# Performance work log

Measured on AMD Instinct MI355X. Metric: run time of the kernel, lower is better.

The kernel has to match this reference:

```python
import jax, jax.numpy as jnp
import numpy as np

EPS = 1e-5

def _ln(x, g, b):
    mu = jnp.mean(x, axis=-1, keepdims=True)
    var = jnp.mean(jnp.square(x - mu), axis=-1, keepdims=True)
    return (x - mu) * jax.lax.rsqrt(var + EPS) * g + b

def setup_inputs() -> dict:
    BS, LN, FS = 64, 256, 512
    H, OUT, ATT, L = 1024, 128, 256, 8
    key = jax.random.key(0)
    ks = jax.random.split(key, 8)
    s = 0.02
    inp = {
        "x": jax.random.normal(ks[0], (BS, LN, FS), jnp.float32),
        # fc stem
        "ln0_g": jnp.ones((FS,), jnp.float32),
        "ln0_b": jnp.zeros((FS,), jnp.float32),
        "W0": jax.random.normal(ks[1], (FS, H), jnp.float32) * s,
        "b0": jnp.zeros((H,), jnp.float32),
        # residual blocks (stacked)
        "res_ln_g": jnp.ones((L, H), jnp.float32),
        "res_ln_b": jnp.zeros((L, H), jnp.float32),
        "res_W": jax.random.normal(ks[2], (L, H, H), jnp.float32) * s,
        "res_b": jnp.zeros((L, H), jnp.float32),
        # fc head
        "lnf_g": jnp.ones((H,), jnp.float32),
        "lnf_b": jnp.zeros((H,), jnp.float32),
        "Wf": jax.random.normal(ks[3], (H, OUT), jnp.float32) * s,
        "bf": jnp.zeros((OUT,), jnp.float32),
        # attention MLP over time axis
        "a_ln1_g": jnp.ones((LN + 1,), jnp.float32),
        "a_ln1_b": jnp.zeros((LN + 1,), jnp.float32),
        "Wa1": jax.random.normal(ks[4], (LN + 1, ATT), jnp.float32) * s,
        "ba1": jnp.zeros((ATT,), jnp.float32),
        "a_ln2_g": jnp.ones((ATT,), jnp.float32),
        "a_ln2_b": jnp.zeros((ATT,), jnp.float32),
        "Wa2": jax.random.normal(ks[5], (ATT, LN), jnp.float32) * s,
        "ba2": jnp.zeros((LN,), jnp.float32),
    }
    return inp

def reference(x, ln0_g, ln0_b, W0, b0, res_ln_g, res_ln_b, res_W, res_b,
              lnf_g, lnf_b, Wf, bf, a_ln1_g, a_ln1_b, Wa1, ba1,
              a_ln2_g, a_ln2_b, Wa2, ba2):
    # fc trunk (dropout is identity in eval)
    h = jax.nn.relu(_ln(x, ln0_g, ln0_b) @ W0 + b0)          # [bs, ln, H]
    for i in range(res_W.shape[0]):
        h = h + jax.nn.relu(_ln(h, res_ln_g[i], res_ln_b[i]) @ res_W[i] + res_b[i])
    fc_out = _ln(h, lnf_g, lnf_b) @ Wf + bf                  # [bs, ln, out]

    # attention: batched over (bs, out) instead of python loop
    mean = jnp.mean(fc_out, axis=1, keepdims=True)           # [bs, 1, out]
    t = jnp.concatenate([fc_out, mean], axis=1).transpose(0, 2, 1)  # [bs, out, ln+1]
    a = jax.nn.relu(_ln(t, a_ln1_g, a_ln1_b) @ Wa1 + ba1)    # [bs, out, att]
    w = _ln(a, a_ln2_g, a_ln2_b) @ Wa2 + ba2                 # [bs, out, ln]
    w = jax.nn.softmax(w, axis=2).transpose(0, 2, 1)         # [bs, ln, out]

    # einsum('ijk,ijk->ik')
    return jnp.sum(fc_out * w, axis=1)                        # [bs, out]
```

## Files before the change

### kernel.cpp

```cpp
#include <hip/hip_runtime.h>
#include <hip/hip_bf16.h>
#include <stdint.h>

#define EPSV 1e-5f

typedef int i32x4 __attribute__((ext_vector_type(4)));

#define QINV_X 15.875f
#define SA_X   0.062992126f
#define QINV_H 5.2916667f
#define SA_H   0.188976378f

__device__ __forceinline__ void gload_lds16(const void* g, void* l) {
    __builtin_amdgcn_global_load_lds(
        (const __attribute__((address_space(1))) uint32_t*)g,
        (__attribute__((address_space(3))) uint32_t*)l, 16, 0, 0);
}

__device__ __forceinline__ float block_sum256(float v, float* red) {
#pragma unroll
    for (int off = 32; off; off >>= 1) v += __shfl_down(v, off);
    int lane = threadIdx.x & 63, w = threadIdx.x >> 6;
    __syncthreads();
    if (lane == 0) red[w] = v;
    __syncthreads();
    return red[0] + red[1] + red[2] + red[3];
}

__global__ __launch_bounds__(256)
void pack_x0(const float* __restrict__ X, uint8_t* __restrict__ Aq,
             float* __restrict__ S0, int D) {
    __shared__ float red[4];
    int row = blockIdx.x;
    const float* x = X + (size_t)row * D;
    int tid = threadIdx.x;
    int nvec = D >> 2;

    float s = 0.f, sq = 0.f;
    for (int i = tid; i < nvec; i += 256) {
        float4 v = ((const float4*)x)[i];
        s += v.x + v.y + v.z + v.w;
        sq += v.x * v.x + v.y * v.y + v.z * v.z + v.w * v.w;
    }
    float ts = block_sum256(s, red);
    float tq = block_sum256(sq, red);
    if (tid == 0) { S0[2 * row] = ts; S0[2 * row + 1] = tq; }

    uint8_t* arow = Aq + (size_t)row * ((size_t)D * 2);
    for (int i = tid; i < nvec; i += 256) {
        float4 v = ((const float4*)x)[i];
        float vals[4] = { v.x, v.y, v.z, v.w };
        uint32_t u1 = 0, u2 = 0;
#pragma unroll
        for (int j = 0; j < 4; ++j) {
            float qv = vals[j] * QINV_X;
            float q1 = rintf(qv);
            q1 = fminf(fmaxf(q1, -127.f), 127.f);
            float q2 = fminf(fmaxf(rintf((qv - q1) * 128.f), -127.f), 127.f);
            u1 |= ((uint32_t)((int)q1 & 0xFF)) << (8 * j);
            u2 |= ((uint32_t)((int)q2 & 0xFF)) << (8 * j);
        }
        int kt = i >> 4;
        int o = (i & 15) * 4;
        *(uint32_t*)(arow + kt * 128 + o) = u1;
        *(uint32_t*)(arow + kt * 128 + 64 + o) = u2;
    }
}

__global__ __launch_bounds__(256)
void wprep_part(const float* __restrict__ W, const float* __restrict__ g,
                const float* __restrict__ lb, float* __restrict__ pA,
                float* __restrict__ pC, float* __restrict__ pD, int K, int N) {
    int n = blockIdx.y * 256 + threadIdx.x;
    int kp = blockIdx.x;
    if (n >= N) return;
    int kc = K >> 3, k0 = kp * kc;
    float ma = 0.f, cs = 0.f, ds = 0.f;
    for (int k = k0; k < k0 + kc; ++k) {
        float w = W[(size_t)k * N + n];
        float gw = g[k] * w;
        ma = fmaxf(ma, fabsf(gw));
        cs += gw;
        ds = fmaf(lb[k], w, ds);
    }
    pA[kp * N + n] = ma;
    pC[kp * N + n] = cs;
    pD[kp * N + n] = ds;
}

__global__ __launch_bounds__(256)
void wprep_fin(const float* __restrict__ pA, const float* __restrict__ pC,
               const float* __restrict__ pD, const float* __restrict__ bias,
               float* __restrict__ sB, float* __restrict__ csum,
               float* __restrict__ d, int N) {
    int n = blockIdx.x * 256 + threadIdx.x;
    if (n >= N) return;
    float m = 0.f, cs = 0.f, ds = 0.f;
#pragma unroll
    for (int kp = 0; kp < 8; ++kp) {
        m = fmaxf(m, pA[kp * N + n]);
        cs += pC[kp * N + n];
        ds += pD[kp * N + n];
    }
    m = fmaxf(m, 1e-30f);
    sB[n] = m * (1.f / 127.f);
    csum[n] = cs;
    d[n] = ds + bias[n];
}

__global__ __launch_bounds__(64)
void conv_wq(const float* __restrict__ W, const float* __restrict__ g,
             const float* __restrict__ sB, uint8_t* __restrict__ Wq,
             int K, int N) {
    int n = blockIdx.x * 64 + threadIdx.x;
    int kt = blockIdx.y;
    if (n >= N) return;
    float inv = 1.f / sB[n];
    uint32_t u1[16], u2[16];
#pragma unroll 4
    for (int o = 0; o < 16; ++o) {
        uint32_t a = 0, bq = 0;
#pragma unroll
        for (int j = 0; j < 4; ++j) {
            int k = kt * 64 + o * 4 + j;
            float q = g[k] * W[(size_t)k * N + n] * inv;
            float q1 = rintf(q);
            float q2 = rintf((q - q1) * 128.f);
            a |= ((uint32_t)((int)q1 & 0xFF)) << (8 * j);
            bq |= ((uint32_t)((int)q2 & 0xFF)) << (8 * j);
        }
        u1[o] = a; u2[o] = bq;
    }
    uint8_t* wrow = Wq + (size_t)n * ((size_t)K * 2) + kt * 128;
    uint4* dd = (uint4*)wrow;
    const uint4* p1 = (const uint4*)u1;
    const uint4* p2 = (const uint4*)u2;
    dd[0] = p1[0]; dd[1] = p1[1]; dd[2] = p1[2]; dd[3] = p1[3];
    dd[4] = p2[0]; dd[5] = p2[1]; dd[6] = p2[2]; dd[7] = p2[3];
}

__global__ __launch_bounds__(256)
void wprep_part_rw(const float* __restrict__ rW, const float* __restrict__ g8,
                   const float* __restrict__ lb8, float* __restrict__ pA,
                   float* __restrict__ pC, float* __restrict__ pD) {
    int c = blockIdx.y * 256 + threadIdx.x;
    int kp = blockIdx.x;
    int layer = c >> 10, n = c & 1023;
    const float* W = rW + ((size_t)layer << 20);
    const float* g = g8 + layer * 1024;
    const float* lb = lb8 + layer * 1024;
    int k0 = kp * 128;
    float ma = 0.f, cs = 0.f, ds = 0.f;
    for (int k = k0; k < k0 + 128; ++k) {
        float w = W[(size_t)k * 1024 + n];
        float gw = g[k] * w;
        ma = fmaxf(ma, fabsf(gw));
        cs += gw;
        ds = fmaf(lb[k], w, ds);
    }
    pA[kp * 8192 + c] = ma;
    pC[kp * 8192 + c] = cs;
    pD[kp * 8192 + c] = ds;
}

__global__ __launch_bounds__(256)
void wprep_fin_rw(const float* __restrict__ pA, const float* __restrict__ pC,
                  const float* __restrict__ pD, const float* __restrict__ rb,
                  float* __restrict__ sB, float* __restrict__ csum,
                  float* __restrict__ d) {
    int c = blockIdx.x * 256 + threadIdx.x;
    float m = 0.f, cs = 0.f, ds = 0.f;
#pragma unroll
    for (int kp = 0; kp < 8; ++kp) {
        m = fmaxf(m, pA[kp * 8192 + c]);
        cs += pC[kp * 8192 + c];
        ds += pD[kp * 8192 + c];
    }
    m = fmaxf(m, 1e-30f);
    sB[c] = m * (1.f / 127.f);
    csum[c] = cs;
    d[c] = ds + rb[c];
}

__global__ __launch_bounds__(64)
void conv_wq_rw(const float* __restrict__ rW, const float* __restrict__ g8,
                const float* __restrict__ sB, uint8_t* __restrict__ Wq) {
    int c = blockIdx.x * 64 + threadIdx.x;
    int kt = blockIdx.y;
    int layer = c >> 10, n = c & 1023;
    const float* W = rW + ((size_t)layer << 20);
    const float* g = g8 + layer * 1024;
    float inv = 1.f / sB[c];
    uint32_t u1[16], u2[16];
#pragma unroll 4
    for (int o = 0; o < 16; ++o) {
        uint32_t a = 0, bq = 0;
#pragma unroll
        for (int j = 0; j < 4; ++j) {
            int k = kt * 64 + o * 4 + j;
            float q = g[k] * W[(size_t)k * 1024 + n] * inv;
            float q1 = rintf(q);
            float q2 = rintf((q - q1) * 128.f);
            a |= ((uint32_t)((int)q1 & 0xFF)) << (8 * j);
            bq |= ((uint32_t)((int)q2 & 0xFF)) << (8 * j);
        }
        u1[o] = a; u2[o] = bq;
    }
    uint8_t* wrow = Wq + ((size_t)layer << 21) + (size_t)n * 2048 + kt * 128;
    uint4* dd = (uint4*)wrow;
    const uint4* p1 = (const uint4*)u1;
    const uint4* p2 = (const uint4*)u2;
    dd[0] = p1[0]; dd[1] = p1[1]; dd[2] = p1[2]; dd[3] = p1[3];
    dd[4] = p2[0]; dd[5] = p2[1]; dd[6] = p2[2]; dd[7] = p2[3];
}

template <int MODE, bool KSPLIT = false>
__global__ __launch_bounds__(512, 4)
void gemm_fold(const uint8_t* __restrict__ Aq, const uint8_t* __restrict__ Bq,
               const float* __restrict__ sB, const float* __restrict__ csum,
               const float* __restrict__ dvec, const float* __restrict__ Sin,
               float* __restrict__ Sout, uint8_t* __restrict__ AqOut,
               float* __restrict__ C, float SA, int M, int N, int K) {
    __shared__ char Abuf[2][16384];
    __shared__ char Bbuf[2][16384];

    const int tid = threadIdx.x;
    const int lane = tid & 63;
    const int wv = tid >> 6;
    const int wr = wv >> 1;
    const int wc = wv & 1;

    int m0, n0, nt;
    size_t kbyte0;
    float* Cout;
    if constexpr (KSPLIT) {
        m0 = blockIdx.x * 128;
        n0 = 0;
        int half = K >> 1;
        nt = half >> 6;
        kbyte0 = (size_t)blockIdx.y * half * 2;
        Cout = C + (size_t)blockIdx.y * M * N;
    } else {
        int lid = blockIdx.y * gridDim.x + blockIdx.x;
        int nwg = gridDim.x * gridDim.y;
        int chunk = nwg >> 3;
        int swz = (lid & 7) * chunk + (lid >> 3);
        int nIdx = swz % gridDim.y;
        int mIdx = swz / gridDim.y;
        m0 = mIdx * 128; n0 = nIdx * 128;
        nt = K >> 6;
        kbyte0 = 0;
        Cout = C;
    }

    const size_t rowB = (size_t)K * 2;

    int arow[2], aq[2];
#pragma unroll
    for (int i = 0; i < 2; ++i) {
        int s = i * 512 + tid;
        arow[i] = s >> 3;
        aq[i] = (s & 7) ^ (arow[i] & 7);
    }

    i32x4 accP[2][4] = {};
    i32x4 accQ[2][4] = {};

#pragma unroll
    for (int i = 0; i < 2; ++i) {
        gload_lds16((const char*)Aq + (size_t)(m0 + arow[i]) * rowB + kbyte0 + aq[i] * 16,
                    Abuf[0] + (i * 512 + tid) * 16);
        gload_lds16((const char*)Bq + (size_t)(n0 + arow[i]) * rowB + kbyte0 + aq[i] * 16,
                    Bbuf[0] + (i * 512 + tid) * 16);
    }
    __syncthreads();

    int p = 0;
    const int g = lane >> 4;
    const int rr = lane & 15;

    for (int kt = 0; kt < nt; ++kt) {
        if (kt + 1 < nt) {
            const size_t koff = kbyte0 + (size_t)(kt + 1) * 128;
#pragma unroll
            for (int i = 0; i < 2; ++i) {
                gload_lds16((const char*)Aq + (size_t)(m0 + arow[i]) * rowB + koff + aq[i] * 16,
                            Abuf[p ^ 1] + (i * 512 + tid) * 16);
                gload_lds16((const char*)Bq + (size_t)(n0 + arow[i]) * rowB + koff + aq[i] * 16,
                            Bbuf[p ^ 1] + (i * 512 + tid) * 16);
            }
        }

        const char* Ab = Abuf[p];
        const char* Bb = Bbuf[p];

        i32x4 a1[2], b1[4];
#pragma unroll
        for (int m = 0; m < 2; ++m) {
            int rA = wr * 32 + m * 16 + rr;
            a1[m] = *(const i32x4*)(Ab + rA * 128 + ((g ^ (rA & 7)) * 16));
        }
#pragma unroll
        for (int n = 0; n < 4; ++n) {
            int rB = wc * 64 + n * 16 + rr;
            b1[n] = *(const i32x4*)(Bb + rB * 128 + ((g ^ (rB & 7)) * 16));
        }
#pragma unroll
        for (int m = 0; m < 2; ++m)
#pragma unroll
            for (int n = 0; n < 4; ++n)
                accP[m][n] = __builtin_amdgcn_mfma_i32_16x16x64_i8(a1[m], b1[n], accP[m][n], 0, 0, 0);

        {
            i32x4 b2[4];
#pragma unroll
            for (int n = 0; n < 4; ++n) {
                int rB = wc * 64 + n * 16 + rr;
                b2[n] = *(const i32x4*)(Bb + rB * 128 + (((g + 4) ^ (rB & 7)) * 16));
            }
#pragma unroll
            for (int m = 0; m < 2; ++m)
#pragma unroll
                for (int n = 0; n < 4; ++n)
                    accQ[m][n] = __builtin_amdgcn_mfma_i32_16x16x64_i8(a1[m], b2[n], accQ[m][n], 0, 0, 0);
        }
        {
            i32x4 a2[2];
#pragma unroll
            for (int m = 0; m < 2; ++m) {
                int rA = wr * 32 + m * 16 + rr;
                a2[m] = *(const i32x4*)(Ab + rA * 128 + (((g + 4) ^ (rA & 7)) * 16));
            }
#pragma unroll
            for (int m = 0; m < 2; ++m)
#pragma unroll
                for (int n = 0; n < 4; ++n)
                    accQ[m][n] = __builtin_amdgcn_mfma_i32_16x16x64_i8(a2[m], b1[n], accQ[m][n], 0, 0, 0);
        }

        __syncthreads();
        p ^= 1;
    }

    const int rg = lane >> 4;
    const int cl = lane & 15;
    const float invK = 1.f / (float)K;

    float sbv[4], csv[4], dvv[4];
#pragma unroll
    for (int n = 0; n < 4; ++n) {
        int c = n0 + wc * 64 + n * 16 + cl;
        sbv[n] = sB[c] * SA;
        if (KSPLIT && blockIdx.y != 0) { csv[n] = 0.f; dvv[n] = 0.f; }
        else { csv[n] = csum[c]; dvv[n] = dvec[c]; }
    }

#pragma unroll
    for (int m = 0; m < 2; ++m) {
#pragma unroll
        for (int j = 0; j < 4; ++j) {
            int r = m0 + wr * 32 + m * 16 + rg * 4 + j;
            float mu = Sin[2 * r] * invK;
            float var = Sin[2 * r + 1] * invK - mu * mu;
            float rstd = rsqrtf(var + EPSV);
            float rs = 0.f, rq = 0.f;
#pragma unroll
            for (int n = 0; n < 4; ++n) {
                int c = n0 + wc * 64 + n * 16 + cl;
                float accv = (float)accP[m][n][j] + 0.0078125f * (float)accQ[m][n][j];
                float y = rstd * (sbv[n] * accv - mu * csv[n]) + dvv[n];
                if (MODE == 2) {
                    Cout[(size_t)r * N + c] = y;
                } else {
                    float* hp = &C[(size_t)r * N + c];
                    float hn = fmaxf(y, 0.f);
                    if (MODE == 1) hn += *hp;
                    *hp = hn;
                    float qv = hn * QINV_H;
                    float q1 = rintf(qv);
                    q1 = fminf(fmaxf(q1, -127.f), 127.f);
                    float q2 = fminf(fmaxf(rintf((qv - q1) * 128.f), -127.f), 127.f);
                    uint8_t* po = AqOut + (size_t)r * ((size_t)N * 2) + ((c >> 6) << 7) + (c & 63);
                    po[0] = (uint8_t)((int)q1 & 0xFF);
                    po[64] = (uint8_t)((int)q2 & 0xFF);
                    rs += hn;
                    rq += hn * hn;
                }
            }
            if (MODE != 2) {
#pragma unroll
                for (int mm = 1; mm < 16; mm <<= 1) {
                    rs += __shfl_xor(rs, mm);
                    rq += __shfl_xor(rq, mm);
                }
                if (cl == 0) {
                    atomicAdd(&Sout[2 * r], rs);
                    atomicAdd(&Sout[2 * r + 1], rq);
                }
            }
        }
    }
}

template <bool MAXOP>
__device__ __forceinline__ void red8(const float* v, float* out, float (*scr)[4]) {
    int lane = threadIdx.x & 63, wv = threadIdx.x >> 6, tid = threadIdx.x;
#pragma unroll
    for (int oo = 0; oo < 8; ++oo) {
        float r = v[oo];
#pragma unroll
        for (int m = 1; m < 64; m <<= 1) {
            float t = __shfl_xor(r, m);
            r = MAXOP ? fmaxf(r, t) : r + t;
        }
        if (lane == 0) scr[oo][wv] = r;
    }
    __syncthreads();
    if (tid < 8) {
        float a = scr[tid][0], b = scr[tid][1], c = scr[tid][2], d = scr[tid][3];
        out[tid] = MAXOP ? fmaxf(fmaxf(a, b), fmaxf(c, d)) : (a + b + c + d);
    }
    __syncthreads();
}

__global__ __launch_bounds__(256, 4)
void attn_g8(const float* __restrict__ fc01,
             const float* __restrict__ g1, const float* __restrict__ b1,
             const float* __restrict__ Wa1, const float* __restrict__ ba1,
             const float* __restrict__ g2, const float* __restrict__ b2,
             const float* __restrict__ Wa2, const float* __restrict__ ba2,
             float* __restrict__ out) {
    __shared__ float buf[257][12];
    __shared__ float scr[8][4];
    __shared__ float sS[8], sQ[8], sO[8];

    const int R128 = 16384 * 128;
    int bs = blockIdx.x >> 4;
    int o0 = (blockIdx.x & 15) * 8;
    int tid = threadIdx.x;
    int jgrp = tid >> 2;
    int kp = tid & 3;

    float vv[8], tmp[8];
    size_t base = (size_t)(bs * 256 + tid) * 128 + o0;
    const float4* fp0 = (const float4*)(fc01 + base);
    const float4* fp1 = (const float4*)(fc01 + R128 + base);
#pragma unroll
    for (int q = 0; q < 2; ++q) {
        float4 t0 = fp0[q];
        float4 t1 = fp1[q];
        vv[4 * q] = t0.x + t1.x; vv[4 * q + 1] = t0.y + t1.y;
        vv[4 * q + 2] = t0.z + t1.z; vv[4 * q + 3] = t0.w + t1.w;
    }

#pragma unroll
    for (int oo = 0; oo < 8; ++oo) tmp[oo] = vv[oo] * vv[oo];
    red8<false>(vv, sS, scr);
    red8<false>(tmp, sQ, scr);

    float gl = g1[tid], bl = b1[tid];
#pragma unroll
    for (int oo = 0; oo < 8; ++oo) {
        float s = sS[oo], q = sQ[oo];
        float mean = s * (1.f / 256.f);
        float mu = (s + mean) * (1.f / 257.f);
        float var = (q + mean * mean) * (1.f / 257.f) - mu * mu;
        float rstd = rsqrtf(var + EPSV);
        tmp[oo] = (vv[oo] - mu) * rstd * gl + bl;
    }
#pragma unroll
    for (int q = 0; q < 2; ++q)
        *(float4*)&buf[tid][4 * q] = *(float4*)&tmp[4 * q];
    if (tid < 8) {
        int oo = tid;
        float s = sS[oo], q = sQ[oo];
        float mean = s * (1.f / 256.f);
        float mu = (s + mean) * (1.f / 257.f);
        float var = (q + mean * mean) * (1.f / 257.f) - mu * mu;
        float rstd = rsqrtf(var + EPSV);
        buf[256][oo] = (mean - mu) * rstd * g1[256] + b1[256];
    }
    __syncthreads();

    float acc1[8][4] = {};
#pragma unroll 2
    for (int i = 0; i < 64; ++i) {
        int k = 4 * i + kp;
        float4 w4 = *(const float4*)&Wa1[(size_t)k * 256 + jgrp * 4];
        float4 t0 = *(const float4*)&buf[k][0];
        float4 t1 = *(const float4*)&buf[k][4];
        float bv[8] = { t0.x, t0.y, t0.z, t0.w, t1.x, t1.y, t1.z, t1.w };
#pragma unroll
        for (int oo = 0; oo < 8; ++oo) {
            acc1[oo][0] = fmaf(bv[oo], w4.x, acc1[oo][0]);
            acc1[oo][1] = fmaf(bv[oo], w4.y, acc1[oo][1]);
            acc1[oo][2] = fmaf(bv[oo], w4.z, acc1[oo][2]);
            acc1[oo][3] = fmaf(bv[oo], w4.w, acc1[oo][3]);
        }
    }
    if (kp == 0) {
        float4 w4 = *(const float4*)&Wa1[(size_t)256 * 256 + jgrp * 4];
#pragma unroll
        for (int oo = 0; oo < 8; ++oo) {
            float bv = buf[256][oo];
            acc1[oo][0] = fmaf(bv, w4.x, acc1[oo][0]);
            acc1[oo][1] = fmaf(bv, w4.y, acc1[oo][1]);
            acc1[oo][2] = fmaf(bv, w4.z, acc1[oo][2]);
            acc1[oo][3] = fmaf(bv, w4.w, acc1[oo][3]);
        }
    }
    float a_[8];
#pragma unroll
    for (int oo = 0; oo < 8; ++oo) {
#pragma unroll
        for (int jj = 0; jj < 4; ++jj) {
            acc1[oo][jj] += __shfl_xor(acc1[oo][jj], 1);
            acc1[oo][jj] += __shfl_xor(acc1[oo][jj], 2);
        }
        float v01 = (kp & 1) ? acc1[oo][1] : acc1[oo][0];
        float v23 = (kp & 1) ? acc1[oo][3] : acc1[oo][2];
        a_[oo] = (kp & 2) ? v23 : v01;
    }
    float bb = ba1[tid];
#pragma unroll
    for (int oo = 0; oo < 8; ++oo) a_[oo] = fmaxf(a_[oo] + bb, 0.f);

#pragma unroll
    for (int oo = 0; oo < 8; ++oo) tmp[oo] = a_[oo] * a_[oo];
    red8<false>(a_, sS, scr);
    red8<false>(tmp, sQ, scr);

    float g2l = g2[tid], b2l = b2[tid];
#pragma unroll
    for (int oo = 0; oo < 8; ++oo) {
        float mu2 = sS[oo] * (1.f / 256.f);
        float rstd2 = rsqrtf(sQ[oo] * (1.f / 256.f) - mu2 * mu2 + EPSV);
        tmp[oo] = (a_[oo] - mu2) * rstd2 * g2l + b2l;
    }
#pragma unroll
    for (int q = 0; q < 2; ++q)
        *(float4*)&buf[tid][4 * q] = *(float4*)&tmp[4 * q];
    __syncthreads();

    float acc2[8][4] = {};
#pragma unroll 2
    for (int i = 0; i < 64; ++i) {
        int k = 4 * i + kp;
        float4 w4 = *(const float4*)&Wa2[(size_t)k * 256 + jgrp * 4];
        float4 t0 = *(const float4*)&buf[k][0];
        float4 t1 = *(const float4*)&buf[k][4];
        float bv[8] = { t0.x, t0.y, t0.z, t0.w, t1.x, t1.y, t1.z, t1.w };
#pragma unroll
        for (int oo = 0; oo < 8; ++oo) {
            acc2[oo][0] = fmaf(bv[oo], w4.x, acc2[oo][0]);
            acc2[oo][1] = fmaf(bv[oo], w4.y, acc2[oo][1]);
            acc2[oo][2] = fmaf(bv[oo], w4.z, acc2[oo][2]);
            acc2[oo][3] = fmaf(bv[oo], w4.w, acc2[oo][3]);
        }
    }
    float w_[8];
#pragma unroll
    for (int oo = 0; oo < 8; ++oo) {
#pragma unroll
        for (int jj = 0; jj < 4; ++jj) {
            acc2[oo][jj] += __shfl_xor(acc2[oo][jj], 1);
            acc2[oo][jj] += __shfl_xor(acc2[oo][jj], 2);
        }
        float v01 = (kp & 1) ? acc2[oo][1] : acc2[oo][0];
        float v23 = (kp & 1) ? acc2[oo][3] : acc2[oo][2];
        w_[oo] = (kp & 2) ? v23 : v01;
    }
    float bb2 = ba2[tid];
#pragma unroll
    for (int oo = 0; oo < 8; ++oo) w_[oo] += bb2;

    red8<true>(w_, sO, scr);
    float e_[8];
#pragma unroll
    for (int oo = 0; oo < 8; ++oo) e_[oo] = __expf(w_[oo] - sO[oo]);
    red8<false>(e_, sS, scr);
#pragma unroll
    for (int oo = 0; oo < 8; ++oo) tmp[oo] = vv[oo] * e_[oo] / sS[oo];
    red8<false>(tmp, sQ, scr);
    if (tid < 8) out[bs * 128 + o0 + tid] = sQ[tid];
}

extern "C" void kernel_launch(void* const* d_in, const int* in_sizes, int n_in,
                              void* d_out, int out_size, void* d_ws, size_t ws_size,
                              hipStream_t stream) {
    const float* x      = (const float*)d_in[0];
    const float* ln0_g  = (const float*)d_in[1];
    const float* ln0_b  = (const float*)d_in[2];
    const float* W0     = (const float*)d_in[3];
    const float* b0     = (const float*)d_in[4];
    const float* rln_g  = (const float*)d_in[5];
    const float* rln_b  = (const float*)d_in[6];
    const float* rW     = (const float*)d_in[7];
    const float* rb     = (const float*)d_in[8];
    const float* lnf_g  = (const float*)d_in[9];
    const float* lnf_b  = (const float*)d_in[10];
    const float* Wf     = (const float*)d_in[11];
    const float* bf_    = (const float*)d_in[12];
    const float* ln1_g  = (const float*)d_in[13];
    const float* ln1_b  = (const float*)d_in[14];
    const float* Wa1    = (const float*)d_in[15];
    const float* ba1    = (const float*)d_in[16];
    const float* ln2_g  = (const float*)d_in[17];
    const float* ln2_b  = (const float*)d_in[18];
    const float* Wa2    = (const float*)d_in[19];
    const float* ba2    = (const float*)d_in[20];
    float* out = (float*)d_out;

    const size_t R = 16384;
    float*   h    = (float*)d_ws;
    uint8_t* AqX  = (uint8_t*)(h + R * 1024);
    uint8_t* Aq1  = AqX + R * 1024;
    uint8_t* Aq2  = Aq1 + R * 2048;
    float*   fc01 = (float*)(Aq2 + R * 2048);
    uint8_t* Wq0  = (uint8_t*)(fc01 + 2 * R * 128);
    uint8_t* WqR  = Wq0 + (size_t)1024 * 1024;
    uint8_t* Wqf  = WqR + (size_t)8 * 1024 * 2048;
    float*   stats = (float*)(Wqf + (size_t)128 * 2048);
    float*   sB0  = stats + 10 * R * 2;
    float*   cs0  = sB0 + 1024;
    float*   d0   = cs0 + 1024;
    float*   sBR  = d0 + 1024;
    float*   csR  = sBR + 8192;
    float*   dR   = csR + 8192;
    float*   sBf  = dR + 8192;
    float*   csf  = sBf + 128;
    float*   df   = csf + 128;
    float*   pA   = df + 128;
    float*   pC   = pA + 65536;
    float*   pD   = pC + 65536;

    hipMemsetAsync(stats, 0, 10 * R * 2 * sizeof(float), stream);

    wprep_part<<<dim3(8, 4), 256, 0, stream>>>(W0, ln0_g, ln0_b, pA, pC, pD, 512, 1024);
    wprep_fin<<<4, 256, 0, stream>>>(pA, pC, pD, b0, sB0, cs0, d0, 1024);
    conv_wq<<<dim3(16, 8), 64, 0, stream>>>(W0, ln0_g, sB0, Wq0, 512, 1024);

    wprep_part_rw<<<dim3(8, 32), 256, 0, stream>>>(rW, rln_g, rln_b, pA, pC, pD);
    wprep_fin_rw<<<32, 256, 0, stream>>>(pA, pC, pD, rb, sBR, csR, dR);
    conv_wq_rw<<<dim3(128, 16), 64, 0, stream>>>(rW, rln_g, sBR, WqR);

    wprep_part<<<dim3(8, 1), 256, 0, stream>>>(Wf, lnf_g, lnf_b, pA, pC, pD, 1024, 128);
    wprep_fin<<<1, 256, 0, stream>>>(pA, pC, pD, bf_, sBf, csf, df, 128);
    conv_wq<<<dim3(2, 16), 64, 0, stream>>>(Wf, lnf_g, sBf, Wqf, 1024, 128);

    pack_x0<<<R, 256, 0, stream>>>(x, AqX, stats, 512);

    gemm_fold<0><<<dim3(128, 8), 512, 0, stream>>>(
        AqX, Wq0, sB0, cs0, d0, stats, stats + R * 2, Aq1, h, SA_X,
        (int)R, 1024, 512);

    uint8_t* cur = Aq1;
    uint8_t* nxt = Aq2;
    for (int i = 0; i < 8; ++i) {
        gemm_fold<1><<<dim3(128, 8), 512, 0, stream>>>(
            cur, WqR + ((size_t)i << 21), sBR + i * 1024, csR + i * 1024, dR + i * 1024,
            stats + (size_t)(1 + i) * R * 2, stats + (size_t)(2 + i) * R * 2,
            nxt, h, SA_H, (int)R, 1024, 1024);
        uint8_t* t = cur; cur = nxt; nxt = t;
    }

    gemm_fold<2, true><<<dim3(128, 2), 512, 0, stream>>>(
        cur, Wqf, sBf, csf, df, stats + (size_t)9 * R * 2, nullptr, nullptr,
        fc01, SA_H, (int)R, 128, 1024);

    attn_g8<<<64 * 16, 256, 0, stream>>>(fc01, ln1_g, ln1_b, Wa1, ba1,
                                         ln2_g, ln2_b, Wa2, ba2, out);
}
```

Measured before the change: 1.009 ms.

## Move attention MLP GEMMs to int8 split-precision MFMA kernels

Replaces the monolithic fp32 FMA attention kernel with a pipeline: a pre-pass normalizes and quantizes each time-series row to two-level int8 (hi/lo bytes) with per-row scales, then an int8 MFMA GEMM computes the first projection with ReLU. A mid kernel applies the second layernorm and requantizes, a second int8 MFMA GEMM computes the logits, and a post kernel does the softmax-weighted reduction. Attention weights are quantized per column on device. This trades scalar FMA compute for matrix cores, at the cost of extra launches, intermediate global-memory traffic and some quantization error.

```diff
diff --git a/kernel.cpp b/kernel.cpp
--- a/kernel.cpp
+++ b/kernel.cpp
@@ -25,6 +25,25 @@
     if (lane == 0) red[w] = v;
     __syncthreads();
     return red[0] + red[1] + red[2] + red[3];
+}
+
+__device__ __forceinline__ float block_max256(float v, float* red) {
+#pragma unroll
+    for (int off = 32; off; off >>= 1) v = fmaxf(v, __shfl_down(v, off));
+    int lane = threadIdx.x & 63, w = threadIdx.x >> 6;
+    __syncthreads();
+    if (lane == 0) red[w] = v;
+    __syncthreads();
+    return fmaxf(fmaxf(red[0], red[1]), fmaxf(red[2], red[3]));
+}
+
+__device__ __forceinline__ void dq8(float v, float inv, uint8_t& q1o, uint8_t& q2o) {
+    float qv = v * inv;
+    float q1 = rintf(qv);
+    q1 = fminf(fmaxf(q1, -127.f), 127.f);
+    float q2 = fminf(fmaxf(rintf((qv - q1) * 128.f), -127.f), 127.f);
+    q1o = (uint8_t)((int)q1 & 0xFF);
+    q2o = (uint8_t)((int)q2 & 0xFF);
 }
 
 __global__ __launch_bounds__(256)
@@ -53,12 +72,10 @@
         uint32_t u1 = 0, u2 = 0;
 #pragma unroll
         for (int j = 0; j < 4; ++j) {
-            float qv = vals[j] * QINV_X;
-            float q1 = rintf(qv);
-            q1 = fminf(fmaxf(q1, -127.f), 127.f);
-            float q2 = fminf(fmaxf(rintf((qv - q1) * 128.f), -127.f), 127.f);
-            u1 |= ((uint32_t)((int)q1 & 0xFF)) << (8 * j);
-            u2 |= ((uint32_t)((int)q2 & 0xFF)) << (8 * j);
+            uint8_t a, b;
+            dq8(vals[j], QINV_X, a, b);
+            u1 |= ((uint32_t)a) << (8 * j);
+            u2 |= ((uint32_t)b) << (8 * j);
         }
         int kt = i >> 4;
         int o = (i & 15) * 4;
@@ -207,6 +224,63 @@
         u1[o] = a; u2[o] = bq;
     }
     uint8_t* wrow = Wq + ((size_t)layer << 21) + (size_t)n * 2048 + kt * 128;
+    uint4* dd = (uint4*)wrow;
+    const uint4* p1 = (const uint4*)u1;
+    const uint4* p2 = (const uint4*)u2;
+    dd[0] = p1[0]; dd[1] = p1[1]; dd[2] = p1[2]; dd[3] = p1[3];
+    dd[4] = p2[0]; dd[5] = p2[1]; dd[6] = p2[2]; dd[7] = p2[3];
+}
+
+__global__ __launch_bounds__(256)
+void wa_absmax(const float* __restrict__ W, float* __restrict__ part,
+               int K, int N) {
+    int n = blockIdx.y * 256 + threadIdx.x;
+    int kp = blockIdx.x;
+    if (n >= N) return;
+    int kc = (K + 7) >> 3;
+    int k0 = kp * kc;
+    int k1 = min(k0 + kc, K);
+    float m = 0.f;
+    for (int k = k0; k < k1; ++k)
+        m = fmaxf(m, fabsf(W[(size_t)k * N + n]));
+    part[kp * N + n] = m;
+}
+
+__global__ __launch_bounds__(256)
+void col_scale_s(const float* __restrict__ part, float* __restrict__ sB, int N) {
+    int n = blockIdx.x * 256 + threadIdx.x;
+    if (n >= N) return;
+    float m = 0.f;
+#pragma unroll
+    for (int kp = 0; kp < 8; ++kp) m = fmaxf(m, part[kp * N + n]);
+    m = fmaxf(m, 1e-30f);
+    sB[n] = m * (1.f / 127.f);
+}
+
+__global__ __launch_bounds__(64)
+void conv_wq_pad(const float* __restrict__ W, const float* __restrict__ sB,
+                 uint8_t* __restrict__ Wq, int Ktrue, int Kpad, int N) {
+    int n = blockIdx.x * 64 + threadIdx.x;
+    int kt = blockIdx.y;
+    if (n >= N) return;
+    float inv = 1.f / sB[n];
+    uint32_t u1[16], u2[16];
+#pragma unroll 4
+    for (int o = 0; o < 16; ++o) {
+        uint32_t a = 0, bq = 0;
+#pragma unroll
+        for (int j = 0; j < 4; ++j) {
+            int k = kt * 64 + o * 4 + j;
+            float w = (k < Ktrue) ? W[(size_t)k * N + n] : 0.f;
+            float q = w * inv;
+            float q1 = rintf(q);
+            float q2 = rintf((q - q1) * 128.f);
+            a |= ((uint32_t)((int)q1 & 0xFF)) << (8 * j);
+            bq |= ((uint32_t)((int)q2 & 0xFF)) << (8 * j);
+        }
+        u1[o] = a; u2[o] = bq;
+    }
+    uint8_t* wrow = Wq + (size_t)n * ((size_t)Kpad * 2) + kt * 128;
     uint4* dd = (uint4*)wrow;
     const uint4* p1 = (const uint4*)u1;
     const uint4* p2 = (const uint4*)u2;
@@ -402,6 +476,138 @@
     }
 }
 
+template <int MODE>
+__global__ __launch_bounds__(512, 4)
+void gemm_i8(const uint8_t* __restrict__ Aq, const uint8_t* __restrict__ Bq,
+             const float* __restrict__ sA, const float* __restrict__ sB,
+             const float* __restrict__ bias, float* __restrict__ C,
+             int M, int N, int K) {
+    __shared__ char Abuf[2][16384];
+    __shared__ char Bbuf[2][16384];
+
+    const int tid = threadIdx.x;
+    const int lane = tid & 63;
+    const int wv = tid >> 6;
+    const int wr = wv >> 1;
+    const int wc = wv & 1;
+
+    int lid = blockIdx.y * gridDim.x + blockIdx.x;
+    int nwg = gridDim.x * gridDim.y;
+    int chunk = nwg >> 3;
+    int swz = (lid & 7) * chunk + (lid >> 3);
+    int nIdx = swz % gridDim.y;
+    int mIdx = swz / gridDim.y;
+    const int m0 = mIdx * 128, n0 = nIdx * 128;
+    const int nt = K >> 6;
+    const size_t rowB = (size_t)K * 2;
+
+    int arow[2], aq[2];
+#pragma unroll
+    for (int i = 0; i < 2; ++i) {
+        int s = i * 512 + tid;
+        arow[i] = s >> 3;
+        aq[i] = (s & 7) ^ (arow[i] & 7);
+    }
+
+    i32x4 accP[2][4] = {};
+    i32x4 accQ[2][4] = {};
+
+#pragma unroll
+    for (int i = 0; i < 2; ++i) {
+        gload_lds16((const char*)Aq + (size_t)(m0 + arow[i]) * rowB + aq[i] * 16,
+                    Abuf[0] + (i * 512 + tid) * 16);
+        gload_lds16((const char*)Bq + (size_t)(n0 + arow[i]) * rowB + aq[i] * 16,
+                    Bbuf[0] + (i * 512 + tid) * 16);
+    }
+    __syncthreads();
+
+    int p = 0;
+    const int g = lane >> 4;
+    const int rr = lane & 15;
+
+    for (int kt = 0; kt < nt; ++kt) {
+        if (kt + 1 < nt) {
+            const size_t koff = (size_t)(kt + 1) * 128;
+#pragma unroll
+            for (int i = 0; i < 2; ++i) {
+                gload_lds16((const char*)Aq + (size_t)(m0 + arow[i]) * rowB + koff + aq[i] * 16,
+                            Abuf[p ^ 1] + (i * 512 + tid) * 16);
+                gload_lds16((const char*)Bq + (size_t)(n0 + arow[i]) * rowB + koff + aq[i] * 16,
+                            Bbuf[p ^ 1] + (i * 512 + tid) * 16);
+            }
+        }
+
+        const char* Ab = Abuf[p];
+        const char* Bb = Bbuf[p];
+
+        i32x4 a1[2], b1[4];
+#pragma unroll
+        for (int m = 0; m < 2; ++m) {
+            int rA = wr * 32 + m * 16 + rr;
+            a1[m] = *(const i32x4*)(Ab + rA * 128 + ((g ^ (rA & 7)) * 16));
+        }
+#pragma unroll
+        for (int n = 0; n < 4; ++n) {
+            int rB = wc * 64 + n * 16 + rr;
+            b1[n] = *(const i32x4*)(Bb + rB * 128 + ((g ^ (rB & 7)) * 16));
+        }
+#pragma unroll
+        for (int m = 0; m < 2; ++m)
+#pragma unroll
+            for (int n = 0; n < 4; ++n)
+                accP[m][n] = __builtin_amdgcn_mfma_i32_16x16x64_i8(a1[m], b1[n], accP[m][n], 0, 0, 0);
+
+        {
+            i32x4 b2[4];
+#pragma unroll
+            for (int n = 0; n < 4; ++n) {
+                int rB = wc * 64 + n * 16 + rr;
+                b2[n] = *(const i32x4*)(Bb + rB * 128 + (((g + 4) ^ (rB & 7)) * 16));
+            }
+#pragma unroll
+            for (int m = 0; m < 2; ++m)
+#pragma unroll
+                for (int n = 0; n < 4; ++n)
+                    accQ[m][n] = __builtin_amdgcn_mfma_i32_16x16x64_i8(a1[m], b2[n], accQ[m][n], 0, 0, 0);
+        }
+        {
+            i32x4 a2[2];
+#pragma unroll
+            for (int m = 0; m < 2; ++m) {
+                int rA = wr * 32 + m * 16 + rr;
+                a2[m] = *(const i32x4*)(Ab + rA * 128 + (((g + 4) ^ (rA & 7)) * 16));
+            }
+#pragma unroll
+            for (int m = 0; m < 2; ++m)
+#pragma unroll
+                for (int n = 0; n < 4; ++n)
+                    accQ[m][n] = __builtin_amdgcn_mfma_i32_16x16x64_i8(a2[m], b1[n], accQ[m][n], 0, 0, 0);
+        }
+
+        __syncthreads();
+        p ^= 1;
+    }
+
+#pragma unroll
+    for (int m = 0; m < 2; ++m) {
+        int rbase = m0 + wr * 32 + m * 16 + (lane >> 4) * 4;
+#pragma unroll
+        for (int n = 0; n < 4; ++n) {
+            int c = n0 + wc * 64 + n * 16 + (lane & 15);
+            float sbc = sB[c];
+            float bv = bias[c];
+#pragma unroll
+            for (int j = 0; j < 4; ++j) {
+                int r = rbase + j;
+                float v = sA[r] * sbc *
+                          ((float)accP[m][n][j] + 0.0078125f * (float)accQ[m][n][j]) + bv;
+                if (MODE == 0) v = fmaxf(v, 0.f);
+                C[(size_t)r * N + c] = v;
+            }
+        }
+    }
+}
+
 template <bool MAXOP>
 __device__ __forceinline__ void red8(const float* v, float* out, float (*scr)[4]) {
     int lane = threadIdx.x & 63, wv = threadIdx.x >> 6, tid = threadIdx.x;
@@ -423,25 +629,21 @@
     __syncthreads();
 }
 
-__global__ __launch_bounds__(256, 4)
-void attn_g8(const float* __restrict__ fc01,
-             const float* __restrict__ g1, const float* __restrict__ b1,
-             const float* __restrict__ Wa1, const float* __restrict__ ba1,
-             const float* __restrict__ g2, const float* __restrict__ b2,
-             const float* __restrict__ Wa2, const float* __restrict__ ba2,
-             float* __restrict__ out) {
-    __shared__ float buf[257][12];
+__global__ __launch_bounds__(256)
+void attn_pre(const float* __restrict__ fc01,
+              const float* __restrict__ g1, const float* __restrict__ b1,
+              uint8_t* __restrict__ AqT, float* __restrict__ sTn) {
     __shared__ float scr[8][4];
     __shared__ float sS[8], sQ[8], sO[8];
+    __shared__ float t256[8];
 
     const int R128 = 16384 * 128;
     int bs = blockIdx.x >> 4;
     int o0 = (blockIdx.x & 15) * 8;
     int tid = threadIdx.x;
-    int jgrp = tid >> 2;
-    int kp = tid & 3;
-
-    float vv[8], tmp[8];
+    int rbase = bs * 128 + o0;
+
+    float vv[8], tn[8], tmp[8];
     size_t base = (size_t)(bs * 256 + tid) * 128 + o0;
     const float4* fp0 = (const float4*)(fc01 + base);
     const float4* fp1 = (const float4*)(fc01 + R128 + base);
@@ -466,11 +668,9 @@
         float mu = (s + mean) * (1.f / 257.f);
         float var = (q + mean * mean) * (1.f / 257.f) - mu * mu;
         float rstd = rsqrtf(var + EPSV);
-        tmp[oo] = (vv[oo] - mu) * rstd * gl + bl;
-    }
-#pragma unroll
-    for (int q = 0; q < 2; ++q)
-        *(float4*)&buf[tid][4 * q] = *(float4*)&tmp[4 * q];
+        tn[oo] = (vv[oo] - mu) * rstd * gl + bl;
+        tmp[oo] = fabsf(tn[oo]);
+    }
     if (tid < 8) {
         int oo = tid;
         float s = sS[oo], q = sQ[oo];
@@ -478,111 +678,95 @@
         float mu = (s + mean) * (1.f / 257.f);
         float var = (q + mean * mean) * (1.f / 257.f) - mu * mu;
         float rstd = rsqrtf(var + EPSV);
-        buf[256][oo] = (mean - mu) * rstd * g1[256] + b1[256];
+        t256[oo] = (mean - mu) * rstd * g1[256] + b1[256];
+    }
+    red8<true>(tmp, sO, scr);
+    if (tid < 8) {
+        sO[tid] = fmaxf(fmaxf(sO[tid], fabsf(t256[tid])), 1e-30f);
+        sTn[rbase + tid] = sO[tid] * (1.f / 127.f);
     }
     __syncthreads();
 
-    float acc1[8][4] = {};
-#pragma unroll 2
-    for (int i = 0; i < 64; ++i) {
-        int k = 4 * i + kp;
-        float4 w4 = *(const float4*)&Wa1[(size_t)k * 256 + jgrp * 4];
-        float4 t0 = *(const float4*)&buf[k][0];
-        float4 t1 = *(const float4*)&buf[k][4];
-        float bv[8] = { t0.x, t0.y, t0.z, t0.w, t1.x, t1.y, t1.z, t1.w };
+#pragma unroll
+    for (int oo = 0; oo < 8; ++oo) {
+        float inv = 127.f / sO[oo];
+        uint8_t q1, q2;
+        dq8(tn[oo], inv, q1, q2);
+        uint8_t* po = AqT + (size_t)(rbase + oo) * 640 + ((tid >> 6) << 7) + (tid & 63);
+        po[0] = q1;
+        po[64] = q2;
+    }
+    if (tid < 64) {
 #pragma unroll
         for (int oo = 0; oo < 8; ++oo) {
-            acc1[oo][0] = fmaf(bv[oo], w4.x, acc1[oo][0]);
-            acc1[oo][1] = fmaf(bv[oo], w4.y, acc1[oo][1]);
-            acc1[oo][2] = fmaf(bv[oo], w4.z, acc1[oo][2]);
-            acc1[oo][3] = fmaf(bv[oo], w4.w, acc1[oo][3]);
-        }
-    }
-    if (kp == 0) {
-        float4 w4 = *(const float4*)&Wa1[(size_t)256 * 256 + jgrp * 4];
-#pragma unroll
-        for (int oo = 0; oo < 8; ++oo) {
-            float bv = buf[256][oo];
-            acc1[oo][0] = fmaf(bv, w4.x, acc1[oo][0]);
-            acc1[oo][1] = fmaf(bv, w4.y, acc1[oo][1]);
-            acc1[oo][2] = fmaf(bv, w4.z, acc1[oo][2]);
-            acc1[oo][3] = fmaf(bv, w4.w, acc1[oo][3]);
-        }
-    }
-    float a_[8];
-#pragma unroll
-    for (int oo = 0; oo < 8; ++oo) {
-#pragma unroll
-        for (int jj = 0; jj < 4; ++jj) {
-            acc1[oo][jj] += __shfl_xor(acc1[oo][jj], 1);
-            acc1[oo][jj] += __shfl_xor(acc1[oo][jj], 2);
-        }
-        float v01 = (kp & 1) ? acc1[oo][1] : acc1[oo][0];
-        float v23 = (kp & 1) ? acc1[oo][3] : acc1[oo][2];
-        a_[oo] = (kp & 2) ? v23 : v01;
-    }
-    float bb = ba1[tid];
-#pragma unroll
-    for (int oo = 0; oo < 8; ++oo) a_[oo] = fmaxf(a_[oo] + bb, 0.f);
-
-#pragma unroll
-    for (int oo = 0; oo < 8; ++oo) tmp[oo] = a_[oo] * a_[oo];
-    red8<false>(a_, sS, scr);
+            uint8_t q1 = 0, q2 = 0;
+            if (tid == 0) dq8(t256[oo], 127.f / sO[oo], q1, q2);
+            uint8_t* po = AqT + (size_t)(rbase + oo) * 640 + 512 + tid;
+            po[0] = q1;
+            po[64] = q2;
+        }
+    }
+}
+
+__global__ __launch_bounds__(256)
+void attn_mid(const float* __restrict__ A, const float* __restrict__ g2,
+              const float* __restrict__ b2, uint8_t* __restrict__ AqM,
+              float* __restrict__ sA2) {
+    __shared__ float red[4];
+    int r = blockIdx.x;
+    int tid = threadIdx.x;
+    float a = A[(size_t)r * 256 + tid];
+    float s = block_sum256(a, red);
+    float q = block_sum256(a * a, red);
+    float mu = s * (1.f / 256.f);
+    float rstd = rsqrtf(q * (1.f / 256.f) - mu * mu + EPSV);
+    float an = (a - mu) * rstd * g2[tid] + b2[tid];
+    float mx = block_max256(fabsf(an), red);
+    mx = fmaxf(mx, 1e-30f);
+    if (tid == 0) sA2[r] = mx * (1.f / 127.f);
+    uint8_t q1, q2;
+    dq8(an, 127.f / mx, q1, q2);
+    uint8_t* po = AqM + (size_t)r * 512 + ((tid >> 6) << 7) + (tid & 63);
+    po[0] = q1;
+    po[64] = q2;
+}
+
+__global__ __launch_bounds__(256)
+void attn_post(const float* __restrict__ fc01, const float* __restrict__ W2,
+               float* __restrict__ out) {
+    __shared__ float scr[8][4];
+    __shared__ float sS[8], sQ[8], sO[8];
+
+    const int R128 = 16384 * 128;
+    int bs = blockIdx.x >> 4;
+    int o0 = (blockIdx.x & 15) * 8;
+    int tid = threadIdx.x;
+    int rbase = bs * 128 + o0;
+
+    float vv[8], wv[8], tmp[8];
+    size_t base = (size_t)(bs * 256 + tid) * 128 + o0;
+    const float4* fp0 = (const float4*)(fc01 + base);
+    const float4* fp1 = (const float4*)(fc01 + R128 + base);
+#pragma unroll
+    for (int q = 0; q < 2; ++q) {
+        float4 t0 = fp0[q];
+        float4 t1 = fp1[q];
+        vv[4 * q] = t0.x + t1.x; vv[4 * q + 1] = t0.y + t1.y;
+        vv[4 * q + 2] = t0.z + t1.z; vv[4 * q + 3] = t0.w + t1.w;
+    }
+#pragma unroll
+    for (int oo = 0; oo < 8; ++oo)
+        wv[oo] = W2[(size_t)(rbase + oo) * 256 + tid];
+
+    red8<true>(wv, sO, scr);
+    float e_[8];
+#pragma unroll
+    for (int oo = 0; oo < 8; ++oo) e_[oo] = __expf(wv[oo] - sO[oo]);
+    red8<false>(e_, sS, scr);
+#pragma unroll
+    for (int oo = 0; oo < 8; ++oo) tmp[oo] = vv[oo] * e_[oo];
     red8<false>(tmp, sQ, scr);
-
-    float g2l = g2[tid], b2l = b2[tid];
-#pragma unroll
-    for (int oo = 0; oo < 8; ++oo) {
-        float mu2 = sS[oo] * (1.f / 256.f);
-        float rstd2 = rsqrtf(sQ[oo] * (1.f / 256.f) - mu2 * mu2 + EPSV);
-        tmp[oo] = (a_[oo] - mu2) * rstd2 * g2l + b2l;
-    }
-#pragma unroll
-    for (int q = 0; q < 2; ++q)
-        *(float4*)&buf[tid][4 * q] = *(float4*)&tmp[4 * q];
-    __syncthreads();
-
-    float acc2[8][4] = {};
-#pragma unroll 2
-    for (int i = 0; i < 64; ++i) {
-        int k = 4 * i + kp;
-        float4 w4 = *(const float4*)&Wa2[(size_t)k * 256 + jgrp * 4];
-        float4 t0 = *(const float4*)&buf[k][0];
-        float4 t1 = *(const float4*)&buf[k][4];
-        float bv[8] = { t0.x, t0.y, t0.z, t0.w, t1.x, t1.y, t1.z, t1.w };
-#pragma unroll
-        for (int oo = 0; oo < 8; ++oo) {
-            acc2[oo][0] = fmaf(bv[oo], w4.x, acc2[oo][0]);
-            acc2[oo][1] = fmaf(bv[oo], w4.y, acc2[oo][1]);
-            acc2[oo][2] = fmaf(bv[oo], w4.z, acc2[oo][2]);
-            acc2[oo][3] = fmaf(bv[oo], w4.w, acc2[oo][3]);
-        }
-    }
-    float w_[8];
-#pragma unroll
-    for (int oo = 0; oo < 8; ++oo) {
-#pragma unroll
-        for (int jj = 0; jj < 4; ++jj) {
-            acc2[oo][jj] += __shfl_xor(acc2[oo][jj], 1);
-            acc2[oo][jj] += __shfl_xor(acc2[oo][jj], 2);
-        }
-        float v01 = (kp & 1) ? acc2[oo][1] : acc2[oo][0];
-        float v23 = (kp & 1) ? acc2[oo][3] : acc2[oo][2];
-        w_[oo] = (kp & 2) ? v23 : v01;
-    }
-    float bb2 = ba2[tid];
-#pragma unroll
-    for (int oo = 0; oo < 8; ++oo) w_[oo] += bb2;
-
-    red8<true>(w_, sO, scr);
-    float e_[8];
-#pragma unroll
-    for (int oo = 0; oo < 8; ++oo) e_[oo] = __expf(w_[oo] - sO[oo]);
-    red8<false>(e_, sS, scr);
-#pragma unroll
-    for (int oo = 0; oo < 8; ++oo) tmp[oo] = vv[oo] * e_[oo] / sS[oo];
-    red8<false>(tmp, sQ, scr);
-    if (tid < 8) out[bs * 128 + o0 + tid] = sQ[tid];
+    if (tid < 8) out[rbase + tid] = sQ[tid] / sS[tid];
 }
 
 extern "C" void kernel_launch(void* const* d_in, const int* in_sizes, int n_in,
@@ -612,6 +796,7 @@
     float* out = (float*)d_out;
 
     const size_t R = 16384;
+    const size_t R2 = 8192;
     float*   h    = (float*)d_ws;
     uint8_t* AqX  = (uint8_t*)(h + R * 1024);
     uint8_t* Aq1  = AqX + R * 1024;
@@ -633,6 +818,17 @@
     float*   pA   = df + 128;
     float*   pC   = pA + 65536;
     float*   pD   = pC + 65536;
+    uint8_t* Wa1q = (uint8_t*)(pD + 65536);
+    uint8_t* Wa2q = Wa1q + (size_t)256 * 640;
+    float*   sB1  = (float*)(Wa2q + (size_t)256 * 512);
+    float*   sB2  = sB1 + 256;
+    float*   pw   = sB2 + 256;
+    float*   a1   = h;
+    float*   w2   = h + R2 * 256;
+    uint8_t* AqT  = (uint8_t*)(h + 2 * R2 * 256);
+    uint8_t* AqM  = AqT + R2 * 640;
+    float*   sTn  = (float*)(AqM + R2 * 512);
+    float*   sA2  = sTn + R2;
 
     hipMemsetAsync(stats, 0, 10 * R * 2 * sizeof(float), stream);
 
@@ -648,8 +844,14 @@
     wprep_fin<<<1, 256, 0, stream>>>(pA, pC, pD, bf_, sBf, csf, df, 128);
     conv_wq<<<dim3(2, 16), 64, 0, stream>>>(Wf, lnf_g, sBf, Wqf, 1024, 128);
 
+    wa_absmax<<<dim3(8, 1), 256, 0, stream>>>(Wa1, pw, 257, 256);
+    col_scale_s<<<1, 256, 0, stream>>>(pw, sB1, 256);
+    conv_wq_pad<<<dim3(4, 5), 64, 0, stream>>>(Wa1, sB1, Wa1q, 257, 320, 256);
+    wa_absmax<<<dim3(8, 1), 256, 0, stream>>>(Wa2, pw, 256, 256);
+    col_scale_s<<<1, 256, 0, stream>>>(pw, sB2, 256);
+    conv_wq_pad<<<dim3(4, 4), 64, 0, stream>>>(Wa2, sB2, Wa2q, 256, 256, 256);
+
     pack_x0<<<R, 256, 0, stream>>>(x, AqX, stats, 512);
-
     gemm_fold<0><<<dim3(128, 8), 512, 0, stream>>>(
         AqX, Wq0, sB0, cs0, d0, stats, stats + R * 2, Aq1, h, SA_X,
         (int)R, 1024, 512);
@@ -668,6 +870,11 @@
         cur, Wqf, sBf, csf, df, stats + (size_t)9 * R * 2, nullptr, nullptr,
         fc01, SA_H, (int)R, 128, 1024);
 
-    attn_g8<<<64 * 16, 256, 0, stream>>>(fc01, ln1_g, ln1_b, Wa1, ba1,
-                                         ln2_g, ln2_b, Wa2, ba2, out);
-}
+    attn_pre<<<64 * 16, 256, 0, stream>>>(fc01, ln1_g, ln1_b, AqT, sTn);
+    gemm_i8<0><<<dim3(64, 2), 512, 0, stream>>>(AqT, Wa1q, sTn, sB1, ba1, a1,
+                                                (int)R2, 256, 320);
+    attn_mid<<<R2, 256, 0, stream>>>(a1, ln2_g, ln2_b, AqM, sA2);
+    gemm_i8<2><<<dim3(64, 2), 512, 0, stream>>>(AqM, Wa2q, sA2, sB2, ba2, w2,
+                                                (int)R2, 256, 256);
+    attn_post<<<64 * 16, 256, 0, stream>>>(fc01, w2, out);
+}
```

New measurement: 996.5 us. About the same (-1.3%).
